# Performance work log

Measured on AMD Instinct MI355X. Metric: run time of the kernel, lower is better.

The kernel has to match this reference:

```python
import jax, jax.numpy as jnp
import numpy as np

EPS = 1e-12  # matches torch F.normalize eps


def _l2norm(v, axis):
    return v / jnp.maximum(jnp.linalg.norm(v, axis=axis, keepdims=True), EPS)


def setup_inputs() -> dict:
    key = jax.random.key(0)
    k1, k2, k3 = jax.random.split(key, 3)
    B, C, H, W, K = 32, 512, 40, 40, 64
    x = jax.random.normal(k1, (B, C, H, W), dtype=jnp.float32)
    centroids = jax.random.uniform(k2, (K, C), dtype=jnp.float32)  # torch.rand init
    assign_w = jax.random.normal(k3, (K, C), dtype=jnp.float32)    # 1x1 conv weight, no bias
    return {"x": x, "centroids": centroids, "assign_w": assign_w}


def reference(x, centroids, assign_w):
    # x: [B, C, H, W]; centroids/assign_w: [K, C]
    B, C, H, W = x.shape
    x = _l2norm(x, axis=1)                      # channel-wise L2 normalize
    xf = x.reshape(B, C, H * W)                 # [B, C, N]
    # 1x1 conv == per-pixel matmul with [K, C] weight
    logits = jnp.einsum('kc,bcn->bkn', assign_w, xf)
    a = jax.nn.softmax(logits, axis=1)          # softmax over clusters, [B, K, N]
    # vlad[b,k,c] = sum_n a[b,k,n] * (x[b,c,n] - centroid[k,c])
    #            = (a @ x^T)[b,k,c] - centroid[k,c] * sum_n a[b,k,n]
    vlad = jnp.einsum('bkn,bcn->bkc', a, xf) - a.sum(axis=-1)[..., None] * centroids[None]
    vlad = _l2norm(vlad, axis=2)                # intra-normalization per cluster
    vlad = vlad.reshape(B, -1)                  # [B, K*C]
    return _l2norm(vlad, axis=1)                # global L2 normalize
```

## Files before the change

kernel.cpp:

```cpp
#include <hip/hip_runtime.h>
#include <hip/hip_bf16.h>
#include <math.h>

#define BB   32
#define CC   512
#define NPIX 1600
#define KK   64
#define NT   25
#define EPSF 1e-12f

typedef __attribute__((ext_vector_type(8))) short bf16x8;
typedef __attribute__((ext_vector_type(4))) float f32x4;
#define MFMA16 __builtin_amdgcn_mfma_f32_16x16x32_bf16

__device__ __forceinline__ ushort f2bf(float f) {
    __hip_bfloat16 h = __float2bfloat16(f);
    return *reinterpret_cast<ushort*>(&h);
}
__device__ __forceinline__ uint pk2bf(float a, float b) {
    return (uint)f2bf(a) | ((uint)f2bf(b) << 16);
}

__global__ __launch_bounds__(256) void k_wprep(const float* __restrict__ w,
                                               ushort* __restrict__ wb) {
    int i = blockIdx.x * 256 + threadIdx.x;
    float2 v = *(const float2*)&w[(size_t)i * 2];
    ((uint*)wb)[i] = pk2bf(v.x, v.y);
}

__global__ __launch_bounds__(256) void k_gemm1m(const float* __restrict__ x,
                                                const ushort* __restrict__ wb,
                                                ushort* __restrict__ a_t,
                                                float* __restrict__ asum_p) {
    int tile = blockIdx.x, b = blockIdx.y;
    int n0 = tile * 64;
    __shared__ __align__(16) ushort Xs[2][64 * 32];
    __shared__ __align__(16) ushort Wsh[2][64 * 32];
    __shared__ __align__(16) float red[16 * 64];
    __shared__ __align__(16) float asw[4 * 64];
    __shared__ __align__(16) float ivs[64];
    int t = threadIdx.x;
    int lane = t & 63, wv = t >> 6;
    int nlo = lane & 15, khi = lane >> 4;
    int sc2 = (t & 15) * 2;
    int sn4 = (t >> 4) * 4;
    int wk  = t >> 2;
    int wc8 = (t & 3) * 8;
    const float* xb = x + (size_t)b * CC * NPIX + n0;
    f32x4 acc[4] = {};
    float ss[4] = {0.f, 0.f, 0.f, 0.f};

    float4 xa, xc; uint4 wp;
    xa = *(const float4*)&xb[(size_t)sc2 * NPIX + sn4];
    xc = *(const float4*)&xb[(size_t)(sc2 + 1) * NPIX + sn4];
    wp = *(const uint4*)&wb[(size_t)wk * CC + wc8];
    {
        uint* XU = (uint*)Xs[0]; uint* WU = (uint*)Wsh[0];
        float va[4] = {xa.x, xa.y, xa.z, xa.w};
        float vc[4] = {xc.x, xc.y, xc.z, xc.w};
#pragma unroll
        for (int j = 0; j < 4; ++j) {
            ss[j] += va[j] * va[j] + vc[j] * vc[j];
            int row = sn4 + j;
            int gp = ((t & 15) >> 2) ^ ((row >> 1) & 3);
            XU[row * 16 + gp * 4 + (t & 3)] = pk2bf(va[j], vc[j]);
        }
        int gp = (t & 3) ^ ((wk >> 1) & 3);
        *(uint4*)&WU[wk * 16 + gp * 4] = wp;
    }
    __syncthreads();

    int cur = 0;
    for (int it = 0; it < 16; ++it) {
        bool pre = (it < 15);
        if (pre) {
            int c0 = (it + 1) * 32;
            xa = *(const float4*)&xb[(size_t)(c0 + sc2) * NPIX + sn4];
            xc = *(const float4*)&xb[(size_t)(c0 + sc2 + 1) * NPIX + sn4];
            wp = *(const uint4*)&wb[(size_t)wk * CC + c0 + wc8];
        }
        {
            const ushort* Xc = Xs[cur];
            const ushort* Wc = Wsh[cur];
            int rn = wv * 16 + nlo;
            int gB = khi ^ ((rn >> 1) & 3);
            bf16x8 bfr = *(const bf16x8*)&Xc[rn * 32 + gB * 8];
#pragma unroll
            for (int kf = 0; kf < 4; ++kf) {
                int rk = kf * 16 + nlo;
                int gA = khi ^ ((rk >> 1) & 3);
                bf16x8 afr = *(const bf16x8*)&Wc[rk * 32 + gA * 8];
                acc[kf] = MFMA16(afr, bfr, acc[kf], 0, 0, 0);
            }
        }
        if (pre) {
            uint* XU = (uint*)Xs[cur ^ 1]; uint* WU = (uint*)Wsh[cur ^ 1];
            float va[4] = {xa.x, xa.y, xa.z, xa.w};
            float vc[4] = {xc.x, xc.y, xc.z, xc.w};
#pragma unroll
            for (int j = 0; j < 4; ++j) {
                ss[j] += va[j] * va[j] + vc[j] * vc[j];
                int row = sn4 + j;
                int gp = ((t & 15) >> 2) ^ ((row >> 1) & 3);
                XU[row * 16 + gp * 4 + (t & 3)] = pk2bf(va[j], vc[j]);
            }
            int gp = (t & 3) ^ ((wk >> 1) & 3);
            *(uint4*)&WU[wk * 16 + gp * 4] = wp;
        }
        __syncthreads();
        cur ^= 1;
    }

#pragma unroll
    for (int j = 0; j < 4; ++j) red[(t & 15) * 64 + sn4 + j] = ss[j];
    __syncthreads();
    if (t < 64) {
        float s = 0.f;
#pragma unroll
        for (int i = 0; i < 16; ++i) s += red[i * 64 + t];
        ivs[t] = 1.f / fmaxf(sqrtf(s), EPSF);
    }
    __syncthreads();

    int nloc = wv * 16 + nlo;
    float invl = ivs[nloc];

    float lv[4][4];
    float mm = -1e30f;
#pragma unroll
    for (int kf = 0; kf < 4; ++kf)
#pragma unroll
        for (int r = 0; r < 4; ++r) {
            lv[kf][r] = acc[kf][r] * invl;
            mm = fmaxf(mm, lv[kf][r]);
        }
    mm = fmaxf(mm, __shfl_xor(mm, 16));
    mm = fmaxf(mm, __shfl_xor(mm, 32));
    float ev[4][4], s = 0.f;
#pragma unroll
    for (int kf = 0; kf < 4; ++kf)
#pragma unroll
        for (int r = 0; r < 4; ++r) {
            ev[kf][r] = expf(lv[kf][r] - mm);
            s += ev[kf][r];
        }
    s += __shfl_xor(s, 16);
    s += __shfl_xor(s, 32);
    float sd = 1.f / s;

    float av[4][4];
#pragma unroll
    for (int kf = 0; kf < 4; ++kf)
#pragma unroll
        for (int r = 0; r < 4; ++r) av[kf][r] = ev[kf][r] * sd;
#pragma unroll
    for (int off = 1; off < 16; off <<= 1)
#pragma unroll
        for (int kf = 0; kf < 4; ++kf)
#pragma unroll
            for (int r = 0; r < 4; ++r) av[kf][r] += __shfl_xor(av[kf][r], off);
    if (nlo == 0) {
#pragma unroll
        for (int kf = 0; kf < 4; ++kf)
#pragma unroll
            for (int r = 0; r < 4; ++r)
                asw[wv * 64 + kf * 16 + khi * 4 + r] = av[kf][r];
    }

    ushort* ab = a_t + (size_t)b * KK * NPIX;
#pragma unroll
    for (int kf = 0; kf < 4; ++kf)
#pragma unroll
        for (int r = 0; r < 4; ++r) {
            int k = kf * 16 + khi * 4 + r;
            ab[(size_t)k * NPIX + n0 + nloc] = f2bf(ev[kf][r] * sd * invl);
        }
    __syncthreads();
    if (t < 64) {
        float a4 = asw[t] + asw[64 + t] + asw[128 + t] + asw[192 + t];
        asum_p[((size_t)b * KK + t) * NT + tile] = a4;
    }
}

__global__ __launch_bounds__(256) void k_vladm(const ushort* __restrict__ a_t,
                                               const float* __restrict__ x,
                                               float* __restrict__ part,
                                               int nchunk) {
    int c0 = blockIdx.x * 64;
    int s  = blockIdx.y;
    int b  = blockIdx.z;
    int t = threadIdx.x, lane = t & 63, wv = t >> 6;
    int clo = lane & 15, nhi = lane >> 4;
    int rc = wv * 16 + clo;
    const ushort* ab = a_t + (size_t)b * KK * NPIX;
    const float*  xr = x + (size_t)b * CC * NPIX + (size_t)(c0 + rc) * NPIX;
    f32x4 acc[4] = {};
    int nbase = s * nchunk, niters = nchunk / 32;

    for (int it = 0; it < niters; ++it) {
        int nb = nbase + it * 32 + nhi * 8;
        float4 x0 = *(const float4*)&xr[nb];
        float4 x1 = *(const float4*)&xr[nb + 4];
        uint4 bp;
        bp.x = pk2bf(x0.x, x0.y); bp.y = pk2bf(x0.z, x0.w);
        bp.z = pk2bf(x1.x, x1.y); bp.w = pk2bf(x1.z, x1.w);
        bf16x8 bfr = *reinterpret_cast<bf16x8*>(&bp);
#pragma unroll
        for (int kf = 0; kf < 4; ++kf) {
            int rk = kf * 16 + clo;
            bf16x8 afr = *(const bf16x8*)&ab[(size_t)rk * NPIX + nb];
            acc[kf] = MFMA16(afr, bfr, acc[kf], 0, 0, 0);
        }
    }

#pragma unroll
    for (int kf = 0; kf < 4; ++kf)
#pragma unroll
        for (int r = 0; r < 4; ++r) {
            int k = kf * 16 + nhi * 4 + r;
            part[(((size_t)s * BB + b) * KK + k) * CC + c0 + rc] = acc[kf][r];
        }
}

__global__ __launch_bounds__(256) void k_asum(const float* __restrict__ asum_p,
                                              float* __restrict__ asum) {
    int row = blockIdx.x * 256 + threadIdx.x;
    const float* p = asum_p + (size_t)row * NT;
    float s = 0.f;
#pragma unroll
    for (int i = 0; i < NT; ++i) s += p[i];
    asum[row] = s;
}

__global__ __launch_bounds__(256) void k_intra(const float* __restrict__ part, int ns,
                                               const float* __restrict__ asum,
                                               const float* __restrict__ cent,
                                               float* __restrict__ out,
                                               float* __restrict__ bsum) {
    int row = blockIdx.x;
    int b = row >> 6, k = row & 63;
    int t = threadIdx.x;
    float v0 = 0.f, v1 = 0.f;
    for (int s2 = 0; s2 < ns; ++s2) {
        const float* p = part + (((size_t)s2 * BB + b) * KK + k) * CC;
        v0 += p[t];
        v1 += p[t + 256];
    }
    float as = asum[row];
    v0 -= as * cent[k * CC + t];
    v1 -= as * cent[k * CC + t + 256];
    float ssq = v0 * v0 + v1 * v1;
#pragma unroll
    for (int off = 32; off; off >>= 1) ssq += __shfl_down(ssq, off, 64);
    __shared__ float red[4];
    __shared__ float s_inv;
    if ((t & 63) == 0) red[t >> 6] = ssq;
    __syncthreads();
    if (t == 0) {
        float sm = red[0] + red[1] + red[2] + red[3];
        float inv = 1.f / fmaxf(sqrtf(sm), EPSF);
        s_inv = inv;
        atomicAdd(&bsum[b], sm * inv * inv);
    }
    __syncthreads();
    float inv = s_inv;
    out[(size_t)row * CC + t]       = v0 * inv;
    out[(size_t)row * CC + t + 256] = v1 * inv;
}

__global__ __launch_bounds__(256) void k_scale(float* __restrict__ out,
                                               const float* __restrict__ bsum) {
    int idx = blockIdx.x * 256 + threadIdx.x;
    int b = idx >> 15;
    out[idx] *= 1.f / fmaxf(sqrtf(bsum[b]), EPSF);
}

extern "C" void kernel_launch(void* const* d_in, const int* in_sizes, int n_in,
                              void* d_out, int out_size, void* d_ws, size_t ws_size,
                              hipStream_t stream) {
    const float* x    = (const float*)d_in[0];
    const float* cent = (const float*)d_in[1];
    const float* w    = (const float*)d_in[2];
    float* out = (float*)d_out;

    char* wsb = (char*)d_ws;
    const size_t oa_at   = 0;
    const size_t oa_wb   = oa_at + (size_t)BB * KK * NPIX * 2;
    const size_t oa_ap   = oa_wb + (size_t)KK * CC * 2;
    const size_t oa_as   = oa_ap + (size_t)BB * KK * NT * 4;
    const size_t oa_bsum = oa_as + (size_t)BB * KK * 4;
    const size_t oa_part = oa_bsum + 128;
    ushort* a_t   = (ushort*)(wsb + oa_at);
    ushort* wb    = (ushort*)(wsb + oa_wb);
    float* asum_p = (float*)(wsb + oa_ap);
    float* asum   = (float*)(wsb + oa_as);
    float* bsum   = (float*)(wsb + oa_bsum);

    const size_t pbytes = (size_t)BB * KK * CC * 4;
    int ns = 0;
    const int cand[3] = {5, 2, 1};
    for (int i = 0; i < 3; ++i) {
        if (oa_part + (size_t)cand[i] * pbytes <= ws_size) { ns = cand[i]; break; }
    }
    float* part = (ns > 0) ? (float*)(wsb + oa_part) : out;
    if (ns == 0) ns = 1;
    int nchunk = NPIX / ns;

    hipMemsetAsync(bsum, 0, BB * sizeof(float), stream);

    k_wprep <<<dim3((KK * CC / 2) / 256), 256, 0, stream>>>(w, wb);
    k_gemm1m<<<dim3(NT, BB), 256, 0, stream>>>(x, wb, a_t, asum_p);
    k_vladm <<<dim3(CC / 64, ns, BB), 256, 0, stream>>>(a_t, x, part, nchunk);
    k_asum  <<<dim3(BB * KK / 256), 256, 0, stream>>>(asum_p, asum);
    k_intra <<<dim3(BB * KK), 256, 0, stream>>>(part, ns, asum, cent, out, bsum);
    k_scale <<<dim3((BB * KK * CC) / 256), 256, 0, stream>>>(out, bsum);
}
```

Before: 104.0 us.

## Stage k_vladm operands through double-buffered swizzled LDS with register prefetch

The VLAD matmul kernel now loads the assignment and x tiles cooperatively into shared memory with an XOR swizzle. It double-buffers them and prefetches the next tile into registers while MFMAs run on the current one. Before, each wave reloaded all four A fragments straight from global memory on every iteration. The change is meant to hide global latency and cut redundant global traffic, at the cost of a __syncthreads per iteration and extra LDS use.

```diff
diff --git a/kernel.cpp b/kernel.cpp
--- a/kernel.cpp
+++ b/kernel.cpp
@@ -189,36 +189,76 @@
     int c0 = blockIdx.x * 64;
     int s  = blockIdx.y;
     int b  = blockIdx.z;
-    int t = threadIdx.x, lane = t & 63, wv = t >> 6;
-    int clo = lane & 15, nhi = lane >> 4;
-    int rc = wv * 16 + clo;
+    __shared__ __align__(16) ushort Ash[2][64 * 32];
+    __shared__ __align__(16) ushort Xsh[2][64 * 32];
+    int t = threadIdx.x;
+    int lane = t & 63, wv = t >> 6;
+    int sk  = t >> 2;
+    int sn8 = (t & 3) * 8;
     const ushort* ab = a_t + (size_t)b * KK * NPIX;
-    const float*  xr = x + (size_t)b * CC * NPIX + (size_t)(c0 + rc) * NPIX;
+    const float*  xb = x + (size_t)b * CC * NPIX;
     f32x4 acc[4] = {};
-    int nbase = s * nchunk, niters = nchunk / 32;
-
+    int nbase = s * nchunk;
+    int niters = nchunk / 32;
+
+    uint4 ar; float4 x0, x1;
+    ar = *(const uint4*)&ab[(size_t)sk * NPIX + nbase + sn8];
+    x0 = *(const float4*)&xb[(size_t)(c0 + sk) * NPIX + nbase + sn8];
+    x1 = *(const float4*)&xb[(size_t)(c0 + sk) * NPIX + nbase + sn8 + 4];
+    {
+        uint* AU = (uint*)Ash[0]; uint* XU = (uint*)Xsh[0];
+        int gp = (t & 3) ^ ((sk >> 1) & 3);
+        *(uint4*)&AU[sk * 16 + gp * 4] = ar;
+        uint4 xp;
+        xp.x = pk2bf(x0.x, x0.y); xp.y = pk2bf(x0.z, x0.w);
+        xp.z = pk2bf(x1.x, x1.y); xp.w = pk2bf(x1.z, x1.w);
+        *(uint4*)&XU[sk * 16 + gp * 4] = xp;
+    }
+    __syncthreads();
+
+    int cur = 0;
     for (int it = 0; it < niters; ++it) {
-        int nb = nbase + it * 32 + nhi * 8;
-        float4 x0 = *(const float4*)&xr[nb];
-        float4 x1 = *(const float4*)&xr[nb + 4];
-        uint4 bp;
-        bp.x = pk2bf(x0.x, x0.y); bp.y = pk2bf(x0.z, x0.w);
-        bp.z = pk2bf(x1.x, x1.y); bp.w = pk2bf(x1.z, x1.w);
-        bf16x8 bfr = *reinterpret_cast<bf16x8*>(&bp);
-#pragma unroll
-        for (int kf = 0; kf < 4; ++kf) {
-            int rk = kf * 16 + clo;
-            bf16x8 afr = *(const bf16x8*)&ab[(size_t)rk * NPIX + nb];
-            acc[kf] = MFMA16(afr, bfr, acc[kf], 0, 0, 0);
-        }
+        bool pre = (it + 1 < niters);
+        if (pre) {
+            int ng = nbase + (it + 1) * 32;
+            ar = *(const uint4*)&ab[(size_t)sk * NPIX + ng + sn8];
+            x0 = *(const float4*)&xb[(size_t)(c0 + sk) * NPIX + ng + sn8];
+            x1 = *(const float4*)&xb[(size_t)(c0 + sk) * NPIX + ng + sn8 + 4];
+        }
+        {
+            const ushort* Ac = Ash[cur];
+            const ushort* Xc = Xsh[cur];
+            int rc = wv * 16 + (lane & 15);
+            int gB = (lane >> 4) ^ ((rc >> 1) & 3);
+            bf16x8 bfr = *(const bf16x8*)&Xc[rc * 32 + gB * 8];
+#pragma unroll
+            for (int kf = 0; kf < 4; ++kf) {
+                int rk = kf * 16 + (lane & 15);
+                int gA = (lane >> 4) ^ ((rk >> 1) & 3);
+                bf16x8 afr = *(const bf16x8*)&Ac[rk * 32 + gA * 8];
+                acc[kf] = MFMA16(afr, bfr, acc[kf], 0, 0, 0);
+            }
+        }
+        if (pre) {
+            uint* AU = (uint*)Ash[cur ^ 1]; uint* XU = (uint*)Xsh[cur ^ 1];
+            int gp = (t & 3) ^ ((sk >> 1) & 3);
+            *(uint4*)&AU[sk * 16 + gp * 4] = ar;
+            uint4 xp;
+            xp.x = pk2bf(x0.x, x0.y); xp.y = pk2bf(x0.z, x0.w);
+            xp.z = pk2bf(x1.x, x1.y); xp.w = pk2bf(x1.z, x1.w);
+            *(uint4*)&XU[sk * 16 + gp * 4] = xp;
+        }
+        __syncthreads();
+        cur ^= 1;
     }
 
 #pragma unroll
     for (int kf = 0; kf < 4; ++kf)
 #pragma unroll
         for (int r = 0; r < 4; ++r) {
-            int k = kf * 16 + nhi * 4 + r;
-            part[(((size_t)s * BB + b) * KK + k) * CC + c0 + rc] = acc[kf][r];
+            int k = kf * 16 + (lane >> 4) * 4 + r;
+            int c = c0 + wv * 16 + (lane & 15);
+            part[(((size_t)s * BB + b) * KK + k) * CC + c] = acc[kf][r];
         }
 }
 
```

After: 93.47 us. 10.1% less time.
